# Optimization experiments

Hardware: AMD Instinct MI355X
Metric: run time of the kernel (lower is better)

Reference implementation:

```python
import jax, jax.numpy as jnp
import numpy as np

I = 32   # input_dim
H = 64   # hidden_dim


def setup_inputs() -> dict:
    key = jax.random.key(0)
    k_seq, k_wi, k_wh, k_bi, k_bh = jax.random.split(key, 5)
    B, T = 4096, 512
    s = 1.0 / np.sqrt(H)  # PyTorch GRU init range
    return {
        "seq": jax.random.normal(k_seq, (B, T, I), dtype=jnp.float32),
        "W_ih": jax.random.uniform(k_wi, (3 * H, I), minval=-s, maxval=s, dtype=jnp.float32),
        "W_hh": jax.random.uniform(k_wh, (3 * H, H), minval=-s, maxval=s, dtype=jnp.float32),
        "b_ih": jax.random.uniform(k_bi, (3 * H,), minval=-s, maxval=s, dtype=jnp.float32),
        "b_hh": jax.random.uniform(k_bh, (3 * H,), minval=-s, maxval=s, dtype=jnp.float32),
    }


def reference(seq, W_ih, W_hh, b_ih, b_hh):
    # Single-layer GRU (PyTorch gate ordering r, z, n); returns final hidden state (B, H).
    B, T, _ = seq.shape
    # Precompute input projections for all timesteps: (B, T, 3H) -> scan over T.
    x_proj = jnp.einsum('bti,gi->btg', seq, W_ih) + b_ih  # g = 3H
    x_proj = jnp.moveaxis(x_proj, 1, 0)  # (T, B, 3H)

    def step(h, xp):
        hp = h @ W_hh.T + b_hh  # (B, 3H)
        xr, xz, xn = jnp.split(xp, 3, axis=-1)
        hr, hz, hn = jnp.split(hp, 3, axis=-1)
        r = jax.nn.sigmoid(xr + hr)
        z = jax.nn.sigmoid(xz + hz)
        n = jnp.tanh(xn + r * hn)
        h_new = (1.0 - z) * n + z * h
        return h_new, None

    h0 = jnp.zeros((B, H), dtype=seq.dtype)
    h_final, _ = jax.lax.scan(step, h0, x_proj)
    return h_final
```

## Files before the change

### kernel.cpp

```cpp
#include <hip/hip_runtime.h>


#define TSTEPS 512
#define IDIM 32
#define HDIM 64

typedef __bf16 bf16x8 __attribute__((ext_vector_type(8)));
typedef __bf16 bf16x4 __attribute__((ext_vector_type(4)));
typedef float f32x4 __attribute__((ext_vector_type(4)));

#define NLOG2E -1.4426950408889634f
#define TWOLOG2E 2.8853900817779268f

#define LOADPAIR(dst0, dst1, ptr, off)                                     \
    asm volatile("global_load_dwordx4 %0, %2, off offset:%c3\n\t"          \
                 "global_load_dwordx4 %1, %2, off offset:%c4"              \
        : "=&v"(dst0), "=&v"(dst1)                                         \
        : "v"(ptr), "i"(off), "i"((off) + 16));

#define ISSUE_CHUNK(qq, baseT) do {                                        \
    const float* _p = seqRow + (size_t)(baseT) * IDIM;                     \
    LOADPAIR(qq[0][0], qq[0][1], _p, 0)                                    \
    LOADPAIR(qq[1][0], qq[1][1], _p, 128)                                  \
    LOADPAIR(qq[2][0], qq[2][1], _p, 256)                                  \
    LOADPAIR(qq[3][0], qq[3][1], _p, 384)                                  \
} while (0)

#define WAITDEP(qq)                                                        \
    asm volatile("s_waitcnt vmcnt(0)"                                      \
        : "+v"(qq[0][0]), "+v"(qq[0][1]), "+v"(qq[1][0]), "+v"(qq[1][1]), \
          "+v"(qq[2][0]), "+v"(qq[2][1]), "+v"(qq[3][0]), "+v"(qq[3][1]))

#define WG_BARRIER() do {                                                  \
    asm volatile("s_waitcnt lgkmcnt(0)" ::: "memory");                     \
    __builtin_amdgcn_s_barrier();                                          \
} while (0)

__global__ __launch_bounds__(256, 2) void gru_fused_kernel(
    const float* __restrict__ seq, const float* __restrict__ W_ih,
    const float* __restrict__ W_hh, const float* __restrict__ b_ih,
    const float* __restrict__ b_hh, float* __restrict__ out)
{
    __shared__ __bf16 hB[2][16][72];

    const int tid  = threadIdx.x;
    const int w    = tid >> 6;
    const int lane = tid & 63;
    const int l    = lane & 15;
    const int lb   = l & 7;
    const int q    = lane >> 4;
    const int b0   = blockIdx.x * 8;

    for (int i = tid; i < 2 * 16 * 72; i += 256)
        (&hB[0][0][0])[i] = (__bf16)0.0f;

    bf16x8 aH[3][2], aI[3];
    #pragma unroll
    for (int g = 0; g < 3; ++g) {
        const float scl = (g < 2) ? NLOG2E : TWOLOG2E;
        const int row = g * 64 + w * 16 + l;
        #pragma unroll
        for (int kc = 0; kc < 2; ++kc) {
            const float* p = W_hh + row * HDIM + kc * 32 + q * 8;
            #pragma unroll
            for (int j = 0; j < 8; ++j) aH[g][kc][j] = (__bf16)(scl * p[j]);
        }
        const float* pi = W_ih + row * IDIM + q * 8;
        #pragma unroll
        for (int j = 0; j < 8; ++j) aI[g][j] = (__bf16)(scl * pi[j]);
    }

    f32x4 biasR4, biasZ4, biasXN4, biasHN4;
    #pragma unroll
    for (int r = 0; r < 4; ++r) {
        const int g = w * 16 + 4 * q + r;
        biasR4[r]  = NLOG2E * (b_ih[g]      + b_hh[g]);
        biasZ4[r]  = NLOG2E * (b_ih[64 + g] + b_hh[64 + g]);
        biasXN4[r] = TWOLOG2E * b_ih[128 + g];
        biasHN4[r] = TWOLOG2E * b_hh[128 + g];
    }

    float h[4] = {0.f, 0.f, 0.f, 0.f};

    const float* seqRow = seq + ((size_t)(b0 + lb) * TSTEPS) * IDIM + q * 8;

    f32x4 qA[4][2], qB[4][2];
    ISSUE_CHUNK(qA, 0);
    ISSUE_CHUNK(qB, 4);
    WAITDEP(qA);
    WAITDEP(qB);

    WG_BARRIER();

    bf16x8 xb;
    #pragma unroll
    for (int j = 0; j < 4; ++j) {
        xb[j]     = (__bf16)qA[0][0][j];
        xb[4 + j] = (__bf16)qA[0][1][j];
    }
    f32x4 accR  = __builtin_amdgcn_mfma_f32_16x16x32_bf16(aI[0], xb, biasR4, 0, 0, 0);
    f32x4 accZ  = __builtin_amdgcn_mfma_f32_16x16x32_bf16(aI[1], xb, biasZ4, 0, 0, 0);
    f32x4 accXN = __builtin_amdgcn_mfma_f32_16x16x32_bf16(aI[2], xb, biasXN4, 0, 0, 0);

    for (int tc = 0; tc < TSTEPS; tc += 8) {
        #pragma unroll
        for (int s = 0; s < 8; ++s) {
            const int buf = s & 1;

            bf16x8 hb0 = *(const bf16x8*)&hB[buf][l][q * 8];
            bf16x8 hb1 = *(const bf16x8*)&hB[buf][l][32 + q * 8];

            accR = __builtin_amdgcn_mfma_f32_16x16x32_bf16(aH[0][0], hb0, accR, 0, 0, 0);
            accZ = __builtin_amdgcn_mfma_f32_16x16x32_bf16(aH[1][0], hb0, accZ, 0, 0, 0);
            f32x4 accHN = __builtin_amdgcn_mfma_f32_16x16x32_bf16(aH[2][0], hb0, biasHN4, 0, 0, 0);
            accR = __builtin_amdgcn_mfma_f32_16x16x32_bf16(aH[0][1], hb1, accR, 0, 0, 0);
            accZ = __builtin_amdgcn_mfma_f32_16x16x32_bf16(aH[1][1], hb1, accZ, 0, 0, 0);
            accHN = __builtin_amdgcn_mfma_f32_16x16x32_bf16(aH[2][1], hb1, accHN, 0, 0, 0);

            bf16x4 hOut;
            #pragma unroll
            for (int r = 0; r < 4; ++r) {
                const float R  = __builtin_amdgcn_exp2f(accR[r]);
                const float rg = __builtin_amdgcn_rcpf(R + 1.0f);
                const float v2 = __builtin_fmaf(rg, accHN[r], accXN[r]);
                const float U  = __builtin_amdgcn_exp2f(v2);
                const float Z  = __builtin_amdgcn_exp2f(accZ[r]);
                const float num = __builtin_fmaf(U, Z + h[r], h[r] - Z);
                const float den = (U + 1.0f) * (Z + 1.0f);
                h[r] = num * __builtin_amdgcn_rcpf(den);
                hOut[r] = (__bf16)h[r];
            }
            *(bf16x4*)&hB[buf ^ 1][l][w * 16 + 4 * q] = hOut;

            if (s == 3) {
                WAITDEP(qB);
                if (tc + 8 < TSTEPS) ISSUE_CHUNK(qA, tc + 8);
            }
            if (s == 7) {
                WAITDEP(qA);
                if (tc + 12 < TSTEPS) ISSUE_CHUNK(qB, tc + 12);
            }

            {
                const int s1 = s + 1;
                const f32x4* x0 = (s1 < 4) ? &qA[s1 & 3][0]
                                           : (s1 < 8) ? &qB[s1 & 3][0]
                                                      : &qA[0][0];
                bf16x8 xb1;
                #pragma unroll
                for (int j = 0; j < 4; ++j) {
                    xb1[j]     = (__bf16)x0[0][j];
                    xb1[4 + j] = (__bf16)x0[1][j];
                }
                accR  = __builtin_amdgcn_mfma_f32_16x16x32_bf16(aI[0], xb1, biasR4, 0, 0, 0);
                accZ  = __builtin_amdgcn_mfma_f32_16x16x32_bf16(aI[1], xb1, biasZ4, 0, 0, 0);
                accXN = __builtin_amdgcn_mfma_f32_16x16x32_bf16(aI[2], xb1, biasXN4, 0, 0, 0);
            }

            WG_BARRIER();
        }
    }

    if (l < 8) {
        float4 o = {h[0], h[1], h[2], h[3]};
        *(float4*)&out[(size_t)(b0 + l) * HDIM + w * 16 + 4 * q] = o;
    }
}

extern "C" void kernel_launch(void* const* d_in, const int* in_sizes, int n_in,
                              void* d_out, int out_size, void* d_ws, size_t ws_size,
                              hipStream_t stream) {
    const float* seq  = (const float*)d_in[0];
    const float* W_ih = (const float*)d_in[1];
    const float* W_hh = (const float*)d_in[2];
    const float* b_ih = (const float*)d_in[3];
    const float* b_hh = (const float*)d_in[4];
    float* out = (float*)d_out;
    gru_fused_kernel<<<512, 256, 0, stream>>>(seq, W_ih, W_hh, b_ih, b_hh, out);
}
```

Before: 542.2 us.

## Interleave two independent 8-row batch groups per workgroup to hide recurrence latency

Each workgroup now processes 16 batch rows as two independent recurrences (A and B), each with its own LDS hidden-state buffer and input prefetch queues. The grid is halved to 256 blocks, and launch bounds drop to one block per SM. The aim is instruction-level parallelism within a wave: the MFMA and transcendental chains of one group can overlap the other's, and each barrier now covers twice the work. The cost is roughly double the register pressure, lower occupancy, and only 256 workgroups, which may leave compute units idle on a 256-CU part.

```diff
diff --git a/kernel.cpp b/kernel.cpp
--- a/kernel.cpp
+++ b/kernel.cpp
@@ -18,8 +18,8 @@
         : "=&v"(dst0), "=&v"(dst1)                                         \
         : "v"(ptr), "i"(off), "i"((off) + 16));
 
-#define ISSUE_CHUNK(qq, baseT) do {                                        \
-    const float* _p = seqRow + (size_t)(baseT) * IDIM;                     \
+#define ISSUE_CHUNK(qq, rowPtr, baseT) do {                                \
+    const float* _p = rowPtr + (size_t)(baseT) * IDIM;                     \
     LOADPAIR(qq[0][0], qq[0][1], _p, 0)                                    \
     LOADPAIR(qq[1][0], qq[1][1], _p, 128)                                  \
     LOADPAIR(qq[2][0], qq[2][1], _p, 256)                                  \
@@ -36,23 +36,25 @@
     __builtin_amdgcn_s_barrier();                                          \
 } while (0)
 
-__global__ __launch_bounds__(256, 2) void gru_fused_kernel(
+#define MFMA16(a, b, c) __builtin_amdgcn_mfma_f32_16x16x32_bf16(a, b, c, 0, 0, 0)
+
+__global__ __launch_bounds__(256, 1) void gru_fused_kernel(
     const float* __restrict__ seq, const float* __restrict__ W_ih,
     const float* __restrict__ W_hh, const float* __restrict__ b_ih,
     const float* __restrict__ b_hh, float* __restrict__ out)
 {
-    __shared__ __bf16 hB[2][16][72];
+    __shared__ __bf16 hA[2][16][72];
+    __shared__ __bf16 hBt[2][16][72];
 
     const int tid  = threadIdx.x;
     const int w    = tid >> 6;
     const int lane = tid & 63;
     const int l    = lane & 15;
-    const int lb   = l & 7;
     const int q    = lane >> 4;
-    const int b0   = blockIdx.x * 8;
-
-    for (int i = tid; i < 2 * 16 * 72; i += 256)
-        (&hB[0][0][0])[i] = (__bf16)0.0f;
+    const int b0   = blockIdx.x * 16;
+
+    for (int i = tid; i < 2 * 16 * 72; i += 256) (&hA[0][0][0])[i]  = (__bf16)0.0f;
+    for (int i = tid; i < 2 * 16 * 72; i += 256) (&hBt[0][0][0])[i] = (__bf16)0.0f;
 
     bf16x8 aH[3][2], aI[3];
     #pragma unroll
@@ -80,81 +82,120 @@
         biasHN4[r] = TWOLOG2E * b_hh[128 + g];
     }
 
-    float h[4] = {0.f, 0.f, 0.f, 0.f};
-
-    const float* seqRow = seq + ((size_t)(b0 + lb) * TSTEPS) * IDIM + q * 8;
-
-    f32x4 qA[4][2], qB[4][2];
-    ISSUE_CHUNK(qA, 0);
-    ISSUE_CHUNK(qB, 4);
-    WAITDEP(qA);
-    WAITDEP(qB);
+    float hA_r[4] = {0.f, 0.f, 0.f, 0.f};
+    float hB_r[4] = {0.f, 0.f, 0.f, 0.f};
+
+    const float* seqRowA = seq + ((size_t)(b0 + (l & 7)) * TSTEPS) * IDIM + q * 8;
+    const float* seqRowB = seq + ((size_t)(b0 + 8 + (l & 7)) * TSTEPS) * IDIM + q * 8;
+
+    f32x4 qAA[4][2], qBA[4][2];
+    f32x4 qAB[4][2], qBB[4][2];
+    ISSUE_CHUNK(qAA, seqRowA, 0);
+    ISSUE_CHUNK(qAB, seqRowB, 0);
+    ISSUE_CHUNK(qBA, seqRowA, 4);
+    ISSUE_CHUNK(qBB, seqRowB, 4);
+    WAITDEP(qAA); WAITDEP(qAB); WAITDEP(qBA); WAITDEP(qBB);
 
     WG_BARRIER();
 
-    bf16x8 xb;
+    bf16x8 xbA, xbB;
     #pragma unroll
     for (int j = 0; j < 4; ++j) {
-        xb[j]     = (__bf16)qA[0][0][j];
-        xb[4 + j] = (__bf16)qA[0][1][j];
-    }
-    f32x4 accR  = __builtin_amdgcn_mfma_f32_16x16x32_bf16(aI[0], xb, biasR4, 0, 0, 0);
-    f32x4 accZ  = __builtin_amdgcn_mfma_f32_16x16x32_bf16(aI[1], xb, biasZ4, 0, 0, 0);
-    f32x4 accXN = __builtin_amdgcn_mfma_f32_16x16x32_bf16(aI[2], xb, biasXN4, 0, 0, 0);
+        xbA[j] = (__bf16)qAA[0][0][j];  xbA[4 + j] = (__bf16)qAA[0][1][j];
+        xbB[j] = (__bf16)qAB[0][0][j];  xbB[4 + j] = (__bf16)qAB[0][1][j];
+    }
+    f32x4 accAR  = MFMA16(aI[0], xbA, biasR4);
+    f32x4 accAZ  = MFMA16(aI[1], xbA, biasZ4);
+    f32x4 accAXN = MFMA16(aI[2], xbA, biasXN4);
+    f32x4 accBR  = MFMA16(aI[0], xbB, biasR4);
+    f32x4 accBZ  = MFMA16(aI[1], xbB, biasZ4);
+    f32x4 accBXN = MFMA16(aI[2], xbB, biasXN4);
 
     for (int tc = 0; tc < TSTEPS; tc += 8) {
         #pragma unroll
         for (int s = 0; s < 8; ++s) {
             const int buf = s & 1;
 
-            bf16x8 hb0 = *(const bf16x8*)&hB[buf][l][q * 8];
-            bf16x8 hb1 = *(const bf16x8*)&hB[buf][l][32 + q * 8];
-
-            accR = __builtin_amdgcn_mfma_f32_16x16x32_bf16(aH[0][0], hb0, accR, 0, 0, 0);
-            accZ = __builtin_amdgcn_mfma_f32_16x16x32_bf16(aH[1][0], hb0, accZ, 0, 0, 0);
-            f32x4 accHN = __builtin_amdgcn_mfma_f32_16x16x32_bf16(aH[2][0], hb0, biasHN4, 0, 0, 0);
-            accR = __builtin_amdgcn_mfma_f32_16x16x32_bf16(aH[0][1], hb1, accR, 0, 0, 0);
-            accZ = __builtin_amdgcn_mfma_f32_16x16x32_bf16(aH[1][1], hb1, accZ, 0, 0, 0);
-            accHN = __builtin_amdgcn_mfma_f32_16x16x32_bf16(aH[2][1], hb1, accHN, 0, 0, 0);
-
-            bf16x4 hOut;
+            bf16x8 a0 = *(const bf16x8*)&hA[buf][l][q * 8];
+            bf16x8 a1 = *(const bf16x8*)&hA[buf][l][32 + q * 8];
+            bf16x8 c0 = *(const bf16x8*)&hBt[buf][l][q * 8];
+            bf16x8 c1 = *(const bf16x8*)&hBt[buf][l][32 + q * 8];
+
+            accAR = MFMA16(aH[0][0], a0, accAR);
+            accAZ = MFMA16(aH[1][0], a0, accAZ);
+            f32x4 accAHN = MFMA16(aH[2][0], a0, biasHN4);
+            accAR = MFMA16(aH[0][1], a1, accAR);
+            accAZ = MFMA16(aH[1][1], a1, accAZ);
+            accAHN = MFMA16(aH[2][1], a1, accAHN);
+
+            accBR = MFMA16(aH[0][0], c0, accBR);
+            accBZ = MFMA16(aH[1][0], c0, accBZ);
+            f32x4 accBHN = MFMA16(aH[2][0], c0, biasHN4);
+            accBR = MFMA16(aH[0][1], c1, accBR);
+            accBZ = MFMA16(aH[1][1], c1, accBZ);
+            accBHN = MFMA16(aH[2][1], c1, accBHN);
+
+            bf16x4 hOutA, hOutB;
             #pragma unroll
             for (int r = 0; r < 4; ++r) {
-                const float R  = __builtin_amdgcn_exp2f(accR[r]);
+                const float R  = __builtin_amdgcn_exp2f(accAR[r]);
                 const float rg = __builtin_amdgcn_rcpf(R + 1.0f);
-                const float v2 = __builtin_fmaf(rg, accHN[r], accXN[r]);
+                const float v2 = __builtin_fmaf(rg, accAHN[r], accAXN[r]);
                 const float U  = __builtin_amdgcn_exp2f(v2);
-                const float Z  = __builtin_amdgcn_exp2f(accZ[r]);
-                const float num = __builtin_fmaf(U, Z + h[r], h[r] - Z);
+                const float Z  = __builtin_amdgcn_exp2f(accAZ[r]);
+                const float num = __builtin_fmaf(U, Z + hA_r[r], hA_r[r] - Z);
                 const float den = (U + 1.0f) * (Z + 1.0f);
-                h[r] = num * __builtin_amdgcn_rcpf(den);
-                hOut[r] = (__bf16)h[r];
-            }
-            *(bf16x4*)&hB[buf ^ 1][l][w * 16 + 4 * q] = hOut;
+                hA_r[r] = num * __builtin_amdgcn_rcpf(den);
+                hOutA[r] = (__bf16)hA_r[r];
+            }
+            #pragma unroll
+            for (int r = 0; r < 4; ++r) {
+                const float R  = __builtin_amdgcn_exp2f(accBR[r]);
+                const float rg = __builtin_amdgcn_rcpf(R + 1.0f);
+                const float v2 = __builtin_fmaf(rg, accBHN[r], accBXN[r]);
+                const float U  = __builtin_amdgcn_exp2f(v2);
+                const float Z  = __builtin_amdgcn_exp2f(accBZ[r]);
+                const float num = __builtin_fmaf(U, Z + hB_r[r], hB_r[r] - Z);
+                const float den = (U + 1.0f) * (Z + 1.0f);
+                hB_r[r] = num * __builtin_amdgcn_rcpf(den);
+                hOutB[r] = (__bf16)hB_r[r];
+            }
+            *(bf16x4*)&hA[buf ^ 1][l][w * 16 + 4 * q]  = hOutA;
+            *(bf16x4*)&hBt[buf ^ 1][l][w * 16 + 4 * q] = hOutB;
 
             if (s == 3) {
-                WAITDEP(qB);
-                if (tc + 8 < TSTEPS) ISSUE_CHUNK(qA, tc + 8);
+                WAITDEP(qBA); WAITDEP(qBB);
+                if (tc + 8 < TSTEPS) {
+                    ISSUE_CHUNK(qAA, seqRowA, tc + 8);
+                    ISSUE_CHUNK(qAB, seqRowB, tc + 8);
+                }
             }
             if (s == 7) {
-                WAITDEP(qA);
-                if (tc + 12 < TSTEPS) ISSUE_CHUNK(qB, tc + 12);
+                WAITDEP(qAA); WAITDEP(qAB);
+                if (tc + 12 < TSTEPS) {
+                    ISSUE_CHUNK(qBA, seqRowA, tc + 12);
+                    ISSUE_CHUNK(qBB, seqRowB, tc + 12);
+                }
             }
 
             {
                 const int s1 = s + 1;
-                const f32x4* x0 = (s1 < 4) ? &qA[s1 & 3][0]
-                                           : (s1 < 8) ? &qB[s1 & 3][0]
-                                                      : &qA[0][0];
-                bf16x8 xb1;
+                const f32x4* xA = (s1 < 4) ? &qAA[s1 & 3][0]
+                                           : (s1 < 8) ? &qBA[s1 & 3][0] : &qAA[0][0];
+                const f32x4* xB = (s1 < 4) ? &qAB[s1 & 3][0]
+                                           : (s1 < 8) ? &qBB[s1 & 3][0] : &qAB[0][0];
+                bf16x8 x1A, x1B;
                 #pragma unroll
                 for (int j = 0; j < 4; ++j) {
-                    xb1[j]     = (__bf16)x0[0][j];
-                    xb1[4 + j] = (__bf16)x0[1][j];
+                    x1A[j] = (__bf16)xA[0][j];  x1A[4 + j] = (__bf16)xA[1][j];
+                    x1B[j] = (__bf16)xB[0][j];  x1B[4 + j] = (__bf16)xB[1][j];
                 }
-                accR  = __builtin_amdgcn_mfma_f32_16x16x32_bf16(aI[0], xb1, biasR4, 0, 0, 0);
-                accZ  = __builtin_amdgcn_mfma_f32_16x16x32_bf16(aI[1], xb1, biasZ4, 0, 0, 0);
-                accXN = __builtin_amdgcn_mfma_f32_16x16x32_bf16(aI[2], xb1, biasXN4, 0, 0, 0);
+                accAR  = MFMA16(aI[0], x1A, biasR4);
+                accAZ  = MFMA16(aI[1], x1A, biasZ4);
+                accAXN = MFMA16(aI[2], x1A, biasXN4);
+                accBR  = MFMA16(aI[0], x1B, biasR4);
+                accBZ  = MFMA16(aI[1], x1B, biasZ4);
+                accBXN = MFMA16(aI[2], x1B, biasXN4);
             }
 
             WG_BARRIER();
@@ -162,8 +203,10 @@
     }
 
     if (l < 8) {
-        float4 o = {h[0], h[1], h[2], h[3]};
-        *(float4*)&out[(size_t)(b0 + l) * HDIM + w * 16 + 4 * q] = o;
+        float4 oA = {hA_r[0], hA_r[1], hA_r[2], hA_r[3]};
+        float4 oB = {hB_r[0], hB_r[1], hB_r[2], hB_r[3]};
+        *(float4*)&out[(size_t)(b0 + l) * HDIM + w * 16 + 4 * q]     = oA;
+        *(float4*)&out[(size_t)(b0 + 8 + l) * HDIM + w * 16 + 4 * q] = oB;
     }
 }
 
@@ -176,5 +219,5 @@
     const float* b_ih = (const float*)d_in[3];
     const float* b_hh = (const float*)d_in[4];
     float* out = (float*)d_out;
-    gru_fused_kernel<<<512, 256, 0, stream>>>(seq, W_ih, W_hh, b_ih, b_hh, out);
+    gru_fused_kernel<<<256, 256, 0, stream>>>(seq, W_ih, W_hh, b_ih, b_hh, out);
 }
```

Result: slower. 634.0 us (+16.9%).
